# Optimization experiments

Measured on AMD Instinct MI355X. Metric: run time of the kernel, lower is better.

Reference implementation:

```python
import jax, jax.numpy as jnp
import numpy as np

N_VISIBLE = 4096
N_HIDDEN = 4096
BATCH = 8192


def setup_inputs() -> dict:
    key = jax.random.key(0)
    k_x, k_w = jax.random.split(key)
    input_data = jax.random.uniform(k_x, (BATCH, N_VISIBLE), dtype=jnp.float32)
    # xavier_uniform with sigmoid gain (=1.0): limit = sqrt(6/(fan_in+fan_out))
    limit = float(np.sqrt(6.0 / (N_VISIBLE + N_HIDDEN)))
    W = jax.random.uniform(k_w, (N_VISIBLE, N_HIDDEN), dtype=jnp.float32,
                           minval=-limit, maxval=limit)
    hidden_bias = jnp.zeros((N_HIDDEN,), dtype=jnp.float32)
    return {"input_data": input_data, "W": W, "hidden_bias": hidden_bias}


def reference(input_data, W, hidden_bias):
    # RBM.sample_hidden_2 (forward): sigmoid(x @ W + b), batched over samples.
    # (The torch code loops per sample with host syncs; same math, vectorized.)
    hid_prob = jax.nn.sigmoid(jnp.matmul(input_data, W) + hidden_bias)
    return hid_prob
```

## Files before the change

kernel.cpp:

```cpp
#include <hip/hip_runtime.h>
#include <cstdint>

#define MDIM 8192
#define NDIM 4096
#define KDIM 4096
#define NT (KDIM / 64)

typedef __bf16 bf16x8 __attribute__((ext_vector_type(8)));
typedef float f32x4 __attribute__((ext_vector_type(4)));

#define MFMA16 __builtin_amdgcn_mfma_f32_16x16x32_bf16

__device__ __forceinline__ void gload_lds16(const void* g, void* l) {
    __builtin_amdgcn_global_load_lds(
        (const __attribute__((address_space(1))) uint32_t*)g,
        (__attribute__((address_space(3))) uint32_t*)l, 16, 0, 0);
}

__device__ __forceinline__ unsigned short bf16_bits(float f) {
    __bf16 b = (__bf16)f;
    return __builtin_bit_cast(unsigned short, b);
}

__device__ __forceinline__ int detect_f32(const void* X) {
    int ok = 1;
    if (threadIdx.x < 128) {
        unsigned short h = ((const unsigned short*)X)[threadIdx.x];
        ok = (h <= 0x3F80);
    }
    return __syncthreads_and(ok) ? 0 : 1;
}

__global__ __launch_bounds__(256) void prep(const void* __restrict__ X,
                                            const void* __restrict__ W,
                                            __bf16* __restrict__ Xb,
                                            __bf16* __restrict__ WT) {
    const int f32 = detect_f32(X);
    const int t = threadIdx.x;
    if (blockIdx.x < 8192) {
        if (!f32) return;
        const float* Xf = (const float*)X;
        const long xbase = (long)blockIdx.x * 4096;
#pragma unroll
        for (int rr = 0; rr < 4; ++rr) {
            const long idx = xbase + rr * 1024 + t * 4;
            float4 v = *(const float4*)(Xf + idx);
            unsigned short r[4] = {bf16_bits(v.x), bf16_bits(v.y),
                                   bf16_bits(v.z), bf16_bits(v.w)};
            *(uint2*)(Xb + idx) = *(const uint2*)r;
        }
        return;
    }
    __shared__ unsigned short tile[64 * 65];
    const int bid = blockIdx.x - 8192;
    const int n0 = (bid & 63) * 64;
    const int k0 = (bid >> 6) * 64;
    if (f32) {
        const float* Wf = (const float*)W;
#pragma unroll
        for (int p = 0; p < 4; ++p) {
            const int ch = p * 256 + t;
            const int kr = ch >> 4;
            const int nc = ch & 15;
            float4 v = *(const float4*)(Wf + (long)(k0 + kr) * NDIM + n0 + nc * 4);
            tile[(nc * 4 + 0) * 65 + kr] = bf16_bits(v.x);
            tile[(nc * 4 + 1) * 65 + kr] = bf16_bits(v.y);
            tile[(nc * 4 + 2) * 65 + kr] = bf16_bits(v.z);
            tile[(nc * 4 + 3) * 65 + kr] = bf16_bits(v.w);
        }
    } else {
        const __bf16* Wb = (const __bf16*)W;
#pragma unroll
        for (int p = 0; p < 2; ++p) {
            const int ch = p * 256 + t;
            const int kr = ch >> 3;
            const int nc = ch & 7;
            uint4 v = *(const uint4*)(Wb + (long)(k0 + kr) * NDIM + n0 + nc * 8);
            const unsigned short* e = (const unsigned short*)&v;
#pragma unroll
            for (int i = 0; i < 8; ++i) tile[(nc * 8 + i) * 65 + kr] = e[i];
        }
    }
    __syncthreads();
#pragma unroll
    for (int p = 0; p < 2; ++p) {
        const int ch = p * 256 + t;
        const int nr = ch >> 3;
        const int kc = ch & 7;
        unsigned short r[8];
#pragma unroll
        for (int i = 0; i < 8; ++i) r[i] = tile[nr * 65 + kc * 8 + i];
        *(uint4*)(WT + (long)(n0 + nr) * KDIM + k0 + kc * 8) = *(uint4*)r;
    }
}

__global__ __launch_bounds__(256) void transpose_w(const void* __restrict__ X,
                                                   const void* __restrict__ W,
                                                   __bf16* __restrict__ WT) {
    __shared__ unsigned short tile[64 * 65];
    const int f32 = detect_f32(X);
    const int t = threadIdx.x;
    const int k0 = blockIdx.y * 64;
    const int n0 = blockIdx.x * 64;
    if (f32) {
        const float* Wf = (const float*)W;
#pragma unroll
        for (int p = 0; p < 4; ++p) {
            const int ch = p * 256 + t;
            const int kr = ch >> 4;
            const int nc = ch & 15;
            float4 v = *(const float4*)(Wf + (long)(k0 + kr) * NDIM + n0 + nc * 4);
            tile[(nc * 4 + 0) * 65 + kr] = bf16_bits(v.x);
            tile[(nc * 4 + 1) * 65 + kr] = bf16_bits(v.y);
            tile[(nc * 4 + 2) * 65 + kr] = bf16_bits(v.z);
            tile[(nc * 4 + 3) * 65 + kr] = bf16_bits(v.w);
        }
    } else {
        const __bf16* Wb = (const __bf16*)W;
#pragma unroll
        for (int p = 0; p < 2; ++p) {
            const int ch = p * 256 + t;
            const int kr = ch >> 3;
            const int nc = ch & 7;
            uint4 v = *(const uint4*)(Wb + (long)(k0 + kr) * NDIM + n0 + nc * 8);
            const unsigned short* e = (const unsigned short*)&v;
#pragma unroll
            for (int i = 0; i < 8; ++i) tile[(nc * 8 + i) * 65 + kr] = e[i];
        }
    }
    __syncthreads();
#pragma unroll
    for (int p = 0; p < 2; ++p) {
        const int ch = p * 256 + t;
        const int nr = ch >> 3;
        const int kc = ch & 7;
        unsigned short r[8];
#pragma unroll
        for (int i = 0; i < 8; ++i) r[i] = tile[nr * 65 + kc * 8 + i];
        *(uint4*)(WT + (long)(n0 + nr) * KDIM + k0 + kc * 8) = *(uint4*)r;
    }
}

#define WAIT_LGKM4()                                       \
    do {                                                   \
        __builtin_amdgcn_sched_barrier(0);                 \
        asm volatile("s_waitcnt lgkmcnt(4)" ::: "memory"); \
        __builtin_amdgcn_sched_barrier(0);                 \
    } while (0)

#define READ_A(dst, paT, q)                                               \
    do {                                                                  \
        dst[0][0] = *(const bf16x8*)((paT) + (2 * (q) + 0) * 1024 + soff0); \
        dst[0][1] = *(const bf16x8*)((paT) + (2 * (q) + 0) * 1024 + soff1); \
        dst[1][0] = *(const bf16x8*)((paT) + (2 * (q) + 1) * 1024 + soff0); \
        dst[1][1] = *(const bf16x8*)((paT) + (2 * (q) + 1) * 1024 + soff1); \
    } while (0)

#define READ_B(pbT)                                           \
    do {                                                      \
        _Pragma("unroll") for (int j = 0; j < 4; ++j) {       \
            bF[j][0] = *(const bf16x8*)((pbT) + j * 1024 + soff0); \
            bF[j][1] = *(const bf16x8*)((pbT) + j * 1024 + soff1); \
        }                                                     \
    } while (0)

#define CLUSTER(aX, q)                                                       \
    do {                                                                     \
        __builtin_amdgcn_s_setprio(1);                                       \
        _Pragma("unroll") for (int kk = 0; kk < 2; ++kk)                     \
            _Pragma("unroll") for (int ii = 0; ii < 2; ++ii)                 \
                _Pragma("unroll") for (int j = 0; j < 4; ++j)                \
                    acc[2 * (q) + ii][j] = MFMA16(aX[ii][kk], bF[j][kk],     \
                                                  acc[2 * (q) + ii][j], 0, 0, 0); \
        __builtin_amdgcn_s_setprio(0);                                       \
    } while (0)

template <int DB>
__device__ __forceinline__ void ktile(const __bf16* pa, const __bf16* pb,
                                      const __bf16* gA, const __bf16* gB,
                                      __bf16* lA, __bf16* lB, long ko2,
                                      int soff0, int soff1, f32x4 (&acc)[8][4],
                                      bf16x8 (&bF)[4][2], bf16x8 (&aP)[2][2],
                                      bf16x8 (&aQ)[2][2]) {
    const __bf16* paT = pa + DB * 16384;
    const __bf16* pbN = pb + (DB ^ 1) * 16384;
    const __bf16* paN = pa + (DB ^ 1) * 16384;
    WAIT_LGKM4();
    CLUSTER(aP, 0);
    READ_A(aP, paT, 2);
    WAIT_LGKM4();
    CLUSTER(aQ, 1);
    READ_A(aQ, paT, 3);
    WAIT_LGKM4();
    CLUSTER(aP, 2);
    __builtin_amdgcn_sched_barrier(0);
    asm volatile("s_waitcnt vmcnt(0) lgkmcnt(0)" ::: "memory");
    __builtin_amdgcn_sched_barrier(0);
    __builtin_amdgcn_s_barrier();
    __builtin_amdgcn_sched_barrier(0);
    gload_lds16(gB + ko2, lB + DB * 16384);
    gload_lds16(gB + (long)64 * KDIM + ko2, lB + DB * 16384 + 4096);
    gload_lds16(gB + (long)128 * KDIM + ko2, lB + DB * 16384 + 8192);
    gload_lds16(gB + (long)192 * KDIM + ko2, lB + DB * 16384 + 12288);
    gload_lds16(gA + ko2, lA + DB * 16384);
    gload_lds16(gA + (long)64 * KDIM + ko2, lA + DB * 16384 + 4096);
    gload_lds16(gA + (long)128 * KDIM + ko2, lA + DB * 16384 + 8192);
    gload_lds16(gA + (long)192 * KDIM + ko2, lA + DB * 16384 + 12288);
    CLUSTER(aQ, 3);
    READ_B(pbN);
    READ_A(aP, paN, 0);
    __builtin_amdgcn_sched_barrier(0);
    READ_A(aQ, paN, 1);
}

__global__ __launch_bounds__(512, 2) void gemm256(
    const void* __restrict__ X, const __bf16* __restrict__ Xb,
    const __bf16* __restrict__ WT, const void* __restrict__ bias,
    void* __restrict__ out) {
    __shared__ __bf16 sA[2][256][64];
    __shared__ __bf16 sB[2][256][64];
    const int f32 = detect_f32(X);
    const __bf16* __restrict__ Abf = f32 ? Xb : (const __bf16*)X;
    const int t = threadIdx.x;
    const int lane = t & 63;
    const int wid = t >> 6;
    const int wm = wid >> 2;
    const int wn = wid & 3;
    const int lrow = lane & 15;
    const int quad = lane >> 4;
    const int l7 = lrow & 7;

    const int flat = blockIdx.x;
    const int swz = (flat & 7) * (512 / 8) + (flat >> 3);
    const long m0 = (long)(swz >> 4) * 256;
    const long n0 = (long)(swz & 15) * 256;

    const int r8 = lane >> 3;
    const int c8 = lane & 7;
    const int cs = (c8 ^ r8) * 8;
    const __bf16* gA = Abf + (m0 + wid * 8 + r8) * KDIM + cs;
    const __bf16* gB = WT + (n0 + wid * 8 + r8) * KDIM + cs;
    __bf16* lA = &sA[0][wid * 8][0];
    __bf16* lB = &sB[0][wid * 8][0];

    const int soff0 = (quad ^ l7) * 8;
    const int soff1 = ((4 + quad) ^ l7) * 8;
    const __bf16* pa = &sA[0][wm * 128 + lrow][0];
    const __bf16* pb = &sB[0][wn * 64 + lrow][0];

    f32x4 acc[8][4] = {};
    bf16x8 bF[4][2], aP[2][2], aQ[2][2];

    gload_lds16(gB, lB);
    gload_lds16(gB + (long)64 * KDIM, lB + 4096);
    gload_lds16(gB + (long)128 * KDIM, lB + 8192);
    gload_lds16(gB + (long)192 * KDIM, lB + 12288);
    gload_lds16(gA, lA);
    gload_lds16(gA + (long)64 * KDIM, lA + 4096);
    gload_lds16(gA + (long)128 * KDIM, lA + 8192);
    gload_lds16(gA + (long)192 * KDIM, lA + 12288);
    gload_lds16(gB + 64, lB + 16384);
    gload_lds16(gB + (long)64 * KDIM + 64, lB + 16384 + 4096);
    gload_lds16(gB + (long)128 * KDIM + 64, lB + 16384 + 8192);
    gload_lds16(gB + (long)192 * KDIM + 64, lB + 16384 + 12288);
    gload_lds16(gA + 64, lA + 16384);
    gload_lds16(gA + (long)64 * KDIM + 64, lA + 16384 + 4096);
    gload_lds16(gA + (long)128 * KDIM + 64, lA + 16384 + 8192);
    gload_lds16(gA + (long)192 * KDIM + 64, lA + 16384 + 12288);
    __builtin_amdgcn_sched_barrier(0);
    asm volatile("s_waitcnt vmcnt(8)" ::: "memory");
    __builtin_amdgcn_sched_barrier(0);
    __builtin_amdgcn_s_barrier();
    __builtin_amdgcn_sched_barrier(0);
    READ_B(pb);
    READ_A(aP, pa, 0);
    __builtin_amdgcn_sched_barrier(0);
    READ_A(aQ, pa, 1);

#pragma unroll 1
    for (int tt = 0; tt < NT; tt += 2) {
        ktile<0>(pa, pb, gA, gB, lA, lB, (long)((tt + 2) & (NT - 1)) * 64,
                 soff0, soff1, acc, bF, aP, aQ);
        ktile<1>(pa, pb, gA, gB, lA, lB, (long)((tt + 3) & (NT - 1)) * 64,
                 soff0, soff1, acc, bF, aP, aQ);
    }

    const int crow0 = (int)m0 + wm * 128 + quad * 4;
    if (f32) {
        float* of = (float*)out;
        const float* bf = (const float*)bias;
#pragma unroll
        for (int j = 0; j < 4; ++j) {
            const int col = (int)n0 + wn * 64 + j * 16 + lrow;
            const float bv = bf[col];
#pragma unroll
            for (int i = 0; i < 8; ++i) {
                const long rbase = (long)(crow0 + i * 16) * NDIM + col;
#pragma unroll
                for (int r = 0; r < 4; ++r) {
                    const float x = acc[i][j][r] + bv;
                    of[rbase + (long)r * NDIM] = 1.0f / (1.0f + __expf(-x));
                }
            }
        }
    } else {
        __bf16* ob = (__bf16*)out;
        const __bf16* bb = (const __bf16*)bias;
#pragma unroll
        for (int j = 0; j < 4; ++j) {
            const int col = (int)n0 + wn * 64 + j * 16 + lrow;
            const float bv = (float)bb[col];
#pragma unroll
            for (int i = 0; i < 8; ++i) {
                const long rbase = (long)(crow0 + i * 16) * NDIM + col;
#pragma unroll
                for (int r = 0; r < 4; ++r) {
                    const float x = acc[i][j][r] + bv;
                    ob[rbase + (long)r * NDIM] = (__bf16)(1.0f / (1.0f + __expf(-x)));
                }
            }
        }
    }
}

template <int MODE>
__global__ __launch_bounds__(256) void gemm_bias_sigmoid(
    const void* __restrict__ X, const __bf16* __restrict__ Xb,
    const void* __restrict__ Wp, const __bf16* __restrict__ WT,
    const void* __restrict__ bias, void* __restrict__ out) {
    __shared__ __bf16 sA[128 * 64];
    __shared__ __bf16 sB[128 * 64];
    const int f32 = detect_f32(X);
    const int t = threadIdx.x;
    const int lane = t & 63;
    const int wid = t >> 6;
    const int m0 = blockIdx.y * 128;
    const int n0 = blockIdx.x * 128;
    const int wm = (wid & 1) * 64;
    const int wn = (wid >> 1) * 64;
    const int lrow = lane & 15;
    const int quad = lane >> 4;

    f32x4 acc[4][4] = {};

    {
        const int srow = t >> 2;
        const int schk = t & 3;
        __bf16* ldsA = sA + wid * 512;
        __bf16* ldsB = sB + wid * 512;
        const int arow = t >> 1;
        const int acol = (t & 1) * 16;
        const int fp = t & 15;
        const int fc = t >> 4;
        uint32_t* sB32 = (uint32_t*)sB;

        auto compute = [&]() {
            bf16x8 aF[4], bFr[4];
            const __bf16* pa = sA + (wm + lrow) * 32 + quad * 8;
            const __bf16* pb = sB + (wn + lrow) * 32 + quad * 8;
#pragma unroll
            for (int i = 0; i < 4; ++i) aF[i] = *(const bf16x8*)(pa + i * 512);
#pragma unroll
            for (int j = 0; j < 4; ++j) bFr[j] = *(const bf16x8*)(pb + j * 512);
#pragma unroll
            for (int i = 0; i < 4; ++i)
#pragma unroll
                for (int j = 0; j < 4; ++j)
                    acc[i][j] = MFMA16(aF[i], bFr[j], acc[i][j], 0, 0, 0);
        };

        if (MODE == 1 && !f32) {
            const __bf16* gA = (const __bf16*)X + (long)(m0 + srow) * KDIM + schk * 8;
            const __bf16* gB = WT + (long)(n0 + srow) * KDIM + schk * 8;
            for (int kt = 0; kt < KDIM / 32; ++kt) {
                const __bf16* a0 = gA + kt * 32;
                gload_lds16(a0, ldsA);
                gload_lds16(a0 + (long)64 * KDIM, ldsA + 2048);
                const __bf16* b0 = gB + kt * 32;
                gload_lds16(b0, ldsB);
                gload_lds16(b0 + (long)64 * KDIM, ldsB + 2048);
                __syncthreads();
                compute();
                __syncthreads();
            }
        } else if (MODE == 1) {
            const float* Xf = (const float*)X;
            const __bf16* gB = WT + (long)(n0 + srow) * KDIM + schk * 8;
            for (int kt = 0; kt < KDIM / 32; ++kt) {
                const __bf16* b0 = gB + kt * 32;
                gload_lds16(b0, ldsB);
                gload_lds16(b0 + (long)64 * KDIM, ldsB + 2048);
                const float* ap = Xf + (long)(m0 + arow) * KDIM + kt * 32 + acol;
                float4 v0 = *(const float4*)(ap);
                float4 v1 = *(const float4*)(ap + 4);
                float4 v2 = *(const float4*)(ap + 8);
                float4 v3 = *(const float4*)(ap + 12);
                unsigned short r[16] = {
                    bf16_bits(v0.x), bf16_bits(v0.y), bf16_bits(v0.z), bf16_bits(v0.w),
                    bf16_bits(v1.x), bf16_bits(v1.y), bf16_bits(v1.z), bf16_bits(v1.w),
                    bf16_bits(v2.x), bf16_bits(v2.y), bf16_bits(v2.z), bf16_bits(v2.w),
                    bf16_bits(v3.x), bf16_bits(v3.y), bf16_bits(v3.z), bf16_bits(v3.w)};
                *(uint4*)(sA + arow * 32 + acol) = *(const uint4*)(r);
                *(uint4*)(sA + arow * 32 + acol + 8) = *(const uint4*)(r + 8);
                __syncthreads();
                compute();
                __syncthreads();
            }
        } else if (MODE == 2 && !f32) {
            const __bf16* gA = (const __bf16*)X + (long)(m0 + srow) * KDIM + schk * 8;
            const __bf16* Wb = (const __bf16*)Wp;
            for (int kt = 0; kt < KDIM / 32; ++kt) {
                const __bf16* a0 = gA + kt * 32;
                gload_lds16(a0, ldsA);
                gload_lds16(a0 + (long)64 * KDIM, ldsA + 2048);
                const __bf16* w0 = Wb + (long)(kt * 32 + 2 * fp) * NDIM + n0 + fc * 8;
                uint4 g0 = *(const uint4*)(w0);
                uint4 g1 = *(const uint4*)(w0 + NDIM);
                const unsigned short* e0 = (const unsigned short*)&g0;
                const unsigned short* e1 = (const unsigned short*)&g1;
#pragma unroll
                for (int i = 0; i < 8; ++i)
                    sB32[(fc * 8 + i) * 16 + fp] =
                        (uint32_t)e0[i] | ((uint32_t)e1[i] << 16);
                __syncthreads();
                compute();
                __syncthreads();
            }
        } else if (MODE == 2) {
            const float* Xf = (const float*)X;
            const float* Wf = (const float*)Wp;
            for (int kt = 0; kt < KDIM / 32; ++kt) {
                const float* ap = Xf + (long)(m0 + arow) * KDIM + kt * 32 + acol;
                float4 v0 = *(const float4*)(ap);
                float4 v1 = *(const float4*)(ap + 4);
                float4 v2 = *(const float4*)(ap + 8);
                float4 v3 = *(const float4*)(ap + 12);
                unsigned short r[16] = {
                    bf16_bits(v0.x), bf16_bits(v0.y), bf16_bits(v0.z), bf16_bits(v0.w),
                    bf16_bits(v1.x), bf16_bits(v1.y), bf16_bits(v1.z), bf16_bits(v1.w),
                    bf16_bits(v2.x), bf16_bits(v2.y), bf16_bits(v2.z), bf16_bits(v2.w),
                    bf16_bits(v3.x), bf16_bits(v3.y), bf16_bits(v3.z), bf16_bits(v3.w)};
                *(uint4*)(sA + arow * 32 + acol) = *(const uint4*)(r);
                *(uint4*)(sA + arow * 32 + acol + 8) = *(const uint4*)(r + 8);
                const float* w0 = Wf + (long)(kt * 32 + 2 * fp) * NDIM + n0 + fc * 8;
                float4 u0 = *(const float4*)(w0);
                float4 u1 = *(const float4*)(w0 + 4);
                float4 u2 = *(const float4*)(w0 + NDIM);
                float4 u3 = *(const float4*)(w0 + NDIM + 4);
                float k0v[8] = {u0.x, u0.y, u0.z, u0.w, u1.x, u1.y, u1.z, u1.w};
                float k1v[8] = {u2.x, u2.y, u2.z, u2.w, u3.x, u3.y, u3.z, u3.w};
#pragma unroll
                for (int i = 0; i < 8; ++i)
                    sB32[(fc * 8 + i) * 16 + fp] =
                        (uint32_t)bf16_bits(k0v[i]) |
                        ((uint32_t)bf16_bits(k1v[i]) << 16);
                __syncthreads();
                compute();
                __syncthreads();
            }
        }
    }

    const int crow = m0 + wm + quad * 4;
    if (f32) {
        float* of = (float*)out;
        const float* bf = (const float*)bias;
#pragma unroll
        for (int j = 0; j < 4; ++j) {
            const int col = n0 + wn + j * 16 + lrow;
            const float bv = bf[col];
#pragma unroll
            for (int i = 0; i < 4; ++i) {
                const long rbase = (long)(crow + i * 16) * NDIM + col;
#pragma unroll
                for (int r = 0; r < 4; ++r) {
                    const float x = acc[i][j][r] + bv;
                    of[rbase + (long)r * NDIM] = 1.0f / (1.0f + __expf(-x));
                }
            }
        }
    } else {
        __bf16* ob = (__bf16*)out;
        const __bf16* bb = (const __bf16*)bias;
#pragma unroll
        for (int j = 0; j < 4; ++j) {
            const int col = n0 + wn + j * 16 + lrow;
            const float bv = (float)bb[col];
#pragma unroll
            for (int i = 0; i < 4; ++i) {
                const long rbase = (long)(crow + i * 16) * NDIM + col;
#pragma unroll
                for (int r = 0; r < 4; ++r) {
                    const float x = acc[i][j][r] + bv;
                    ob[rbase + (long)r * NDIM] = (__bf16)(1.0f / (1.0f + __expf(-x)));
                }
            }
        }
    }
}

extern "C" void kernel_launch(void* const* d_in, const int* in_sizes, int n_in,
                              void* d_out, int out_size, void* d_ws,
                              size_t ws_size, hipStream_t stream) {
    const void* X = d_in[0];
    const void* W = d_in[1];
    const void* bias = d_in[2];

    const size_t wt_bytes = (size_t)KDIM * NDIM * sizeof(__bf16);
    const size_t xb_bytes = (size_t)MDIM * KDIM * sizeof(__bf16);

    if (ws_size >= wt_bytes + xb_bytes) {
        __bf16* WT = (__bf16*)d_ws;
        __bf16* Xb = (__bf16*)((char*)d_ws + wt_bytes);
        prep<<<8192 + 4096, 256, 0, stream>>>(X, W, Xb, WT);
        gemm256<<<dim3((MDIM / 256) * (NDIM / 256)), 512, 0, stream>>>(
            X, Xb, WT, bias, d_out);
    } else if (ws_size >= wt_bytes) {
        __bf16* WT = (__bf16*)d_ws;
        transpose_w<<<dim3(NDIM / 64, KDIM / 64), 256, 0, stream>>>(X, W, WT);
        dim3 gg(NDIM / 128, MDIM / 128);
        gemm_bias_sigmoid<1><<<gg, 256, 0, stream>>>(X, nullptr, W, WT, bias, d_out);
    } else {
        dim3 gg(NDIM / 128, MDIM / 128);
        gemm_bias_sigmoid<2><<<gg, 256, 0, stream>>>(X, nullptr, W, nullptr, bias, d_out);
    }
}
```

Baseline: 529.5 us.

## Restructure GEMM k-loop into ping-pong phases with interleaved split LDS prefetch

Reworks the 256x256 bf16 GEMM main loop into four barrier-delimited phases per k-tile. Each phase reads its A/B fragments from LDS, issues two of the next tile's global-to-LDS loads, and runs one MFMA cluster, so loads are spread across the tile instead of issued in a burst after a full drain. The warp-to-row mapping of A changes so each wave covers two interleaved 64-row halves, with the epilogue row indexing updated to match. Partial vmcnt waits replace the full drain, in exchange for more s_barrier calls per tile and tighter ordering between LDS buffer reuse and in-flight loads.

```diff
diff --git a/kernel.cpp b/kernel.cpp
--- a/kernel.cpp
+++ b/kernel.cpp
@@ -141,76 +141,81 @@
     }
 }
 
-#define WAIT_LGKM4()                                       \
+#define P_OPEN()                                           \
     do {                                                   \
         __builtin_amdgcn_sched_barrier(0);                 \
-        asm volatile("s_waitcnt lgkmcnt(4)" ::: "memory"); \
+        __builtin_amdgcn_s_barrier();                      \
+        asm volatile("s_waitcnt lgkmcnt(0)" ::: "memory"); \
         __builtin_amdgcn_sched_barrier(0);                 \
     } while (0)
-
-#define READ_A(dst, paT, q)                                               \
-    do {                                                                  \
-        dst[0][0] = *(const bf16x8*)((paT) + (2 * (q) + 0) * 1024 + soff0); \
-        dst[0][1] = *(const bf16x8*)((paT) + (2 * (q) + 0) * 1024 + soff1); \
-        dst[1][0] = *(const bf16x8*)((paT) + (2 * (q) + 1) * 1024 + soff0); \
-        dst[1][1] = *(const bf16x8*)((paT) + (2 * (q) + 1) * 1024 + soff1); \
+#define P_CLOSE()                          \
+    do {                                   \
+        __builtin_amdgcn_sched_barrier(0); \
+        __builtin_amdgcn_s_barrier();      \
     } while (0)
 
-#define READ_B(pbT)                                           \
-    do {                                                      \
-        _Pragma("unroll") for (int j = 0; j < 4; ++j) {       \
-            bF[j][0] = *(const bf16x8*)((pbT) + j * 1024 + soff0); \
-            bF[j][1] = *(const bf16x8*)((pbT) + j * 1024 + soff1); \
-        }                                                     \
-    } while (0)
-
-#define CLUSTER(aX, q)                                                       \
+#define CL(Q)                                                                \
     do {                                                                     \
         __builtin_amdgcn_s_setprio(1);                                       \
         _Pragma("unroll") for (int kk = 0; kk < 2; ++kk)                     \
             _Pragma("unroll") for (int ii = 0; ii < 2; ++ii)                 \
                 _Pragma("unroll") for (int j = 0; j < 4; ++j)                \
-                    acc[2 * (q) + ii][j] = MFMA16(aX[ii][kk], bF[j][kk],     \
-                                                  acc[2 * (q) + ii][j], 0, 0, 0); \
+                    acc[2 * (Q) + ii][j] = MFMA16(aF[ii][kk], bF[j][kk],     \
+                                                  acc[2 * (Q) + ii][j], 0, 0, 0); \
         __builtin_amdgcn_s_setprio(0);                                       \
+    } while (0)
+
+#define READ_AQ(OFF)                                          \
+    do {                                                      \
+        aF[0][0] = *(const bf16x8*)(paT + (OFF) + soff0);     \
+        aF[0][1] = *(const bf16x8*)(paT + (OFF) + soff1);     \
+        aF[1][0] = *(const bf16x8*)(paT + (OFF) + 1024 + soff0); \
+        aF[1][1] = *(const bf16x8*)(paT + (OFF) + 1024 + soff1); \
     } while (0)
 
 template <int DB>
 __device__ __forceinline__ void ktile(const __bf16* pa, const __bf16* pb,
                                       const __bf16* gA, const __bf16* gB,
-                                      __bf16* lA, __bf16* lB, long ko2,
-                                      int soff0, int soff1, f32x4 (&acc)[8][4],
-                                      bf16x8 (&bF)[4][2], bf16x8 (&aP)[2][2],
-                                      bf16x8 (&aQ)[2][2]) {
+                                      __bf16* lA, __bf16* lB,
+                                      long ko1, long ko2,
+                                      int soff0, int soff1,
+                                      f32x4 (&acc)[8][4]) {
     const __bf16* paT = pa + DB * 16384;
-    const __bf16* pbN = pb + (DB ^ 1) * 16384;
-    const __bf16* paN = pa + (DB ^ 1) * 16384;
-    WAIT_LGKM4();
-    CLUSTER(aP, 0);
-    READ_A(aP, paT, 2);
-    WAIT_LGKM4();
-    CLUSTER(aQ, 1);
-    READ_A(aQ, paT, 3);
-    WAIT_LGKM4();
-    CLUSTER(aP, 2);
+    const __bf16* pbT = pb + DB * 16384;
+    bf16x8 aF[2][2], bF[4][2];
+#pragma unroll
+    for (int j = 0; j < 4; ++j) {
+        bF[j][0] = *(const bf16x8*)(pbT + j * 1024 + soff0);
+        bF[j][1] = *(const bf16x8*)(pbT + j * 1024 + soff1);
+    }
+    READ_AQ(0);
+    gload_lds16(gA + (long)128 * KDIM + ko1, lA + (DB ^ 1) * 16384 + 8192);
+    gload_lds16(gA + (long)192 * KDIM + ko1, lA + (DB ^ 1) * 16384 + 12288);
+    asm volatile("s_waitcnt lgkmcnt(8)" ::: "memory");
+    P_OPEN();
+    CL(0);
+    P_CLOSE();
+    READ_AQ(2048);
+    gload_lds16(gB + ko2, lB + DB * 16384);
+    gload_lds16(gB + (long)64 * KDIM + ko2, lB + DB * 16384 + 4096);
+    P_OPEN();
+    CL(1);
+    P_CLOSE();
+    READ_AQ(8192);
+    gload_lds16(gA + ko2, lA + DB * 16384);
+    gload_lds16(gA + (long)64 * KDIM + ko2, lA + DB * 16384 + 4096);
+    P_OPEN();
+    CL(2);
+    P_CLOSE();
+    READ_AQ(10240);
+    gload_lds16(gB + (long)128 * KDIM + ko2, lB + DB * 16384 + 8192);
+    gload_lds16(gB + (long)192 * KDIM + ko2, lB + DB * 16384 + 12288);
+    P_OPEN();
+    CL(3);
     __builtin_amdgcn_sched_barrier(0);
-    asm volatile("s_waitcnt vmcnt(0) lgkmcnt(0)" ::: "memory");
+    asm volatile("s_waitcnt vmcnt(6)" ::: "memory");
     __builtin_amdgcn_sched_barrier(0);
     __builtin_amdgcn_s_barrier();
-    __builtin_amdgcn_sched_barrier(0);
-    gload_lds16(gB + ko2, lB + DB * 16384);
-    gload_lds16(gB + (long)64 * KDIM + ko2, lB + DB * 16384 + 4096);
-    gload_lds16(gB + (long)128 * KDIM + ko2, lB + DB * 16384 + 8192);
-    gload_lds16(gB + (long)192 * KDIM + ko2, lB + DB * 16384 + 12288);
-    gload_lds16(gA + ko2, lA + DB * 16384);
-    gload_lds16(gA + (long)64 * KDIM + ko2, lA + DB * 16384 + 4096);
-    gload_lds16(gA + (long)128 * KDIM + ko2, lA + DB * 16384 + 8192);
-    gload_lds16(gA + (long)192 * KDIM + ko2, lA + DB * 16384 + 12288);
-    CLUSTER(aQ, 3);
-    READ_B(pbN);
-    READ_A(aP, paN, 0);
-    __builtin_amdgcn_sched_barrier(0);
-    READ_A(aQ, paN, 1);
 }
 
 __global__ __launch_bounds__(512, 2) void gemm256(
@@ -245,47 +250,38 @@
 
     const int soff0 = (quad ^ l7) * 8;
     const int soff1 = ((4 + quad) ^ l7) * 8;
-    const __bf16* pa = &sA[0][wm * 128 + lrow][0];
+    const __bf16* pa = &sA[0][wm * 64 + lrow][0];
     const __bf16* pb = &sB[0][wn * 64 + lrow][0];
 
     f32x4 acc[8][4] = {};
-    bf16x8 bF[4][2], aP[2][2], aQ[2][2];
 
     gload_lds16(gB, lB);
     gload_lds16(gB + (long)64 * KDIM, lB + 4096);
+    gload_lds16(gA, lA);
+    gload_lds16(gA + (long)64 * KDIM, lA + 4096);
     gload_lds16(gB + (long)128 * KDIM, lB + 8192);
     gload_lds16(gB + (long)192 * KDIM, lB + 12288);
-    gload_lds16(gA, lA);
-    gload_lds16(gA + (long)64 * KDIM, lA + 4096);
     gload_lds16(gA + (long)128 * KDIM, lA + 8192);
     gload_lds16(gA + (long)192 * KDIM, lA + 12288);
     gload_lds16(gB + 64, lB + 16384);
     gload_lds16(gB + (long)64 * KDIM + 64, lB + 16384 + 4096);
+    gload_lds16(gA + 64, lA + 16384);
+    gload_lds16(gA + (long)64 * KDIM + 64, lA + 16384 + 4096);
     gload_lds16(gB + (long)128 * KDIM + 64, lB + 16384 + 8192);
     gload_lds16(gB + (long)192 * KDIM + 64, lB + 16384 + 12288);
-    gload_lds16(gA + 64, lA + 16384);
-    gload_lds16(gA + (long)64 * KDIM + 64, lA + 16384 + 4096);
-    gload_lds16(gA + (long)128 * KDIM + 64, lA + 16384 + 8192);
-    gload_lds16(gA + (long)192 * KDIM + 64, lA + 16384 + 12288);
     __builtin_amdgcn_sched_barrier(0);
-    asm volatile("s_waitcnt vmcnt(8)" ::: "memory");
+    asm volatile("s_waitcnt vmcnt(6)" ::: "memory");
     __builtin_amdgcn_sched_barrier(0);
     __builtin_amdgcn_s_barrier();
-    __builtin_amdgcn_sched_barrier(0);
-    READ_B(pb);
-    READ_A(aP, pa, 0);
-    __builtin_amdgcn_sched_barrier(0);
-    READ_A(aQ, pa, 1);
 
 #pragma unroll 1
     for (int tt = 0; tt < NT; tt += 2) {
-        ktile<0>(pa, pb, gA, gB, lA, lB, (long)((tt + 2) & (NT - 1)) * 64,
-                 soff0, soff1, acc, bF, aP, aQ);
-        ktile<1>(pa, pb, gA, gB, lA, lB, (long)((tt + 3) & (NT - 1)) * 64,
-                 soff0, soff1, acc, bF, aP, aQ);
-    }
-
-    const int crow0 = (int)m0 + wm * 128 + quad * 4;
+        ktile<0>(pa, pb, gA, gB, lA, lB, (long)((tt + 1) & (NT - 1)) * 64,
+                 (long)((tt + 2) & (NT - 1)) * 64, soff0, soff1, acc);
+        ktile<1>(pa, pb, gA, gB, lA, lB, (long)((tt + 2) & (NT - 1)) * 64,
+                 (long)((tt + 3) & (NT - 1)) * 64, soff0, soff1, acc);
+    }
+
     if (f32) {
         float* of = (float*)out;
         const float* bf = (const float*)bias;
@@ -295,7 +291,9 @@
             const float bv = bf[col];
 #pragma unroll
             for (int i = 0; i < 8; ++i) {
-                const long rbase = (long)(crow0 + i * 16) * NDIM + col;
+                const int rr = (int)m0 + (i >> 2) * 128 + wm * 64 +
+                               (i & 3) * 16 + quad * 4;
+                const long rbase = (long)rr * NDIM + col;
 #pragma unroll
                 for (int r = 0; r < 4; ++r) {
                     const float x = acc[i][j][r] + bv;
@@ -312,7 +310,9 @@
             const float bv = (float)bb[col];
 #pragma unroll
             for (int i = 0; i < 8; ++i) {
-                const long rbase = (long)(crow0 + i * 16) * NDIM + col;
+                const int rr = (int)m0 + (i >> 2) * 128 + wm * 64 +
+                               (i & 3) * 16 + quad * 4;
+                const long rbase = (long)rr * NDIM + col;
 #pragma unroll
                 for (int r = 0; r < 4; ++r) {
                     const float x = acc[i][j][r] + bv;
```

After: 527.4 us. About the same (-0.4%).
